# Optimization experiments

Hardware: AMD Instinct MI355X
Metric: run time of the kernel (lower is better)

The kernel has to match this reference:

```python
import jax, jax.numpy as jnp
import numpy as np

B, N, C, R = 16, 1024, 256, 8
E = 262144
NUM_SUPER = 32
EPS = 1e-5


def _ln(x, g, b):
    mu = jnp.mean(x, axis=-1, keepdims=True)
    var = jnp.var(x, axis=-1, keepdims=True)
    return (x - mu) / jnp.sqrt(var + EPS) * g + b


def setup_inputs() -> dict:
    key = jax.random.key(0)
    ks = jax.random.split(key, 20)

    def w(k, shape, fan_in):
        return (jax.random.normal(k, shape, jnp.float32) / np.sqrt(fan_in)).astype(jnp.float32)

    return dict(
        x=jax.random.normal(ks[0], (B, N, C), jnp.float32),
        batch_edge_index=jax.random.randint(ks[1], (2, E), 0, B * N),
        batch_edge_types=jax.random.randint(ks[2], (E,), 0, R),
        # cross-modal attention
        Wq=w(ks[3], (C, C), C), bq=jnp.zeros((C,), jnp.float32),
        Wk=w(ks[4], (C, C), C), bk=jnp.zeros((C,), jnp.float32),
        Wv=w(ks[5], (C, C), C), bv=jnp.zeros((C,), jnp.float32),
        Wg=w(ks[6], (2 * C, C), 2 * C), bg=jnp.zeros((C,), jnp.float32),
        ln_attn_g=jnp.ones((C,), jnp.float32), ln_attn_b=jnp.zeros((C,), jnp.float32),
        # confidence net
        Wc1=w(ks[7], (C, C // 2), C), bc1=jnp.zeros((C // 2,), jnp.float32),
        Wc2=w(ks[8], (C // 2, 1), C // 2), bc2=jnp.zeros((1,), jnp.float32),
        # feature mixer
        Wm=w(ks[9], (2 * C, C), 2 * C), bm=jnp.zeros((C,), jnp.float32),
        ln1_g=jnp.ones((C,), jnp.float32), ln1_b=jnp.zeros((C,), jnp.float32),
        # RGCN
        W_rel=w(ks[10], (R, C, C), C),
        W_root=w(ks[11], (C, C), C),
        b_rgcn=jnp.zeros((C,), jnp.float32),
        ln2_g=jnp.ones((C,), jnp.float32), ln2_b=jnp.zeros((C,), jnp.float32),
        # super class head
        Wh=w(ks[12], (C, NUM_SUPER), C), bh=jnp.zeros((NUM_SUPER,), jnp.float32),
    )


def reference(x, batch_edge_index, batch_edge_types,
              Wq, bq, Wk, bk, Wv, bv, Wg, bg, ln_attn_g, ln_attn_b,
              Wc1, bc1, Wc2, bc2, Wm, bm, ln1_g, ln1_b,
              W_rel, W_root, b_rgcn, ln2_g, ln2_b, Wh, bh):
    residual = x
    q = x @ Wq + bq
    k = x @ Wk + bk
    v = x @ Wv + bv
    attn = jax.nn.softmax(jnp.einsum('bnc,bmc->bnm', q, k) / jnp.sqrt(jnp.float32(C)), axis=-1)
    out = jnp.einsum('bnm,bmc->bnc', attn, v)
    gate = jax.nn.sigmoid(jnp.concatenate([out, residual], axis=-1) @ Wg + bg)
    validated = _ln(gate * out + (1.0 - gate) * residual, ln_attn_g, ln_attn_b)

    conf = jax.nn.sigmoid(jax.nn.relu(validated @ Wc1 + bc1) @ Wc2 + bc2)  # [B,N,1]
    weighted = validated * conf
    xm = jax.nn.relu(jnp.concatenate([x, weighted], axis=-1) @ Wm + bm)
    xn = _ln(xm, ln1_g, ln1_b).reshape(B * N, C)

    # RGCNConv (PyG defaults: mean aggregation per relation, root weight, bias)
    src, dst = batch_edge_index[0], batch_edge_index[1]
    h = jnp.einsum('nc,rcd->rnd', xn, W_rel)          # [R, B*N, C] relation-transformed nodes
    msg = h[batch_edge_types, src]                    # [E, C] per-edge gather
    seg = dst * R + batch_edge_types                  # (node, relation) segment id
    cnt = jax.ops.segment_sum(jnp.ones((E,), xn.dtype), seg, num_segments=B * N * R)
    msg = msg / jnp.maximum(cnt[seg], 1.0)[:, None]
    agg = jax.ops.segment_sum(msg, dst, num_segments=B * N)
    x_rgcn = agg + xn @ W_root + b_rgcn
    x_rgcn = jax.nn.relu(_ln(x_rgcn.reshape(B, N, C), ln2_g, ln2_b))

    denom = jnp.maximum(conf.sum(axis=1), 1e-8)       # [B,1]
    pooled = (x_rgcn * conf).sum(axis=1) / denom      # [B,C]
    return pooled @ Wh + bh                           # [B, NUM_SUPER]
```

## Files before the change

### kernel.cpp

```cpp
#include <hip/hip_runtime.h>
#include <hip/hip_bf16.h>

#define B_ 16
#define N_ 1024
#define C_ 256
#define R_ 8
#define E_ 262144
#define NS_ 32
#define BN_ (B_*N_)
#define BNC_ (BN_*C_)

typedef __hip_bfloat16 bf16;
typedef __attribute__((ext_vector_type(4))) float f32x4;
typedef __attribute__((ext_vector_type(8))) short bf16x8;

__device__ __forceinline__ float b2f(bf16 x) { return __bfloat162float(x); }
__device__ __forceinline__ bf16  f2b(float x) { return __float2bfloat16(x); }
__device__ __forceinline__ float us2f(unsigned short u) { return __uint_as_float((unsigned)u << 16); }

__device__ __forceinline__ void gload16(const void* g, void* l) {
    auto gp = (const __attribute__((address_space(1))) void*)(unsigned long long)g;
    auto lp = (__attribute__((address_space(3))) void*)(unsigned)(unsigned long long)l;
    __builtin_amdgcn_global_load_lds(gp, lp, 16, 0, 0);
}

template<int ACT>
__global__ __launch_bounds__(256) void gemm_bf16(
    const bf16* __restrict__ A, int lda, long long sA,
    const bf16* __restrict__ Bm, int ldb, long long sB,
    bf16* __restrict__ Cc, int ldc, long long sC,
    const float* __restrict__ bias, const float* __restrict__ bias2,
    const float* __restrict__ bias3, int K)
{
    __shared__ short sbuf[16384];
    const int tid = threadIdx.x;
    const int lane = tid & 63, w = tid >> 6;
    const int wr = w >> 1, wc = w & 1;

    const int gx = gridDim.x;
    const int nwg = gx * gridDim.y;
    int id = blockIdx.y * gx + blockIdx.x;
    if ((nwg & 7) == 0) { const int cpx = nwg >> 3; id = (id & 7) * cpx + (id >> 3); }
    const int bm = (id / gx) * 128, bn = (id % gx) * 128;

    const bf16* Ab = A + (size_t)blockIdx.z * sA;
    const bf16* Bb = Bm + (size_t)blockIdx.z * sB;
    bf16* Cb = Cc + (size_t)blockIdx.z * sC;

    const int rg = lane >> 2;
    const int kswz = ((lane & 3) ^ ((rg >> 1) & 3)) * 8;

    f32x4 acc[4][4];
    const f32x4 zz = {0.f, 0.f, 0.f, 0.f};
    #pragma unroll
    for (int i = 0; i < 4; ++i)
        #pragma unroll
        for (int j = 0; j < 4; ++j) acc[i][j] = zz;

    const int fr = lane & 15;
    const int fm = lane >> 4;
    const int fslot = (fm ^ ((fr >> 1) & 3)) * 8;

    const int NI = K >> 5;

#define STAGE_AB(bi, kk) do {                                                          \
    _Pragma("unroll")                                                                  \
    for (int t_ = 0; t_ < 2; ++t_) {                                                   \
        gload16(Ab + (size_t)(bm + t_*64 + w*16 + rg) * lda + (kk) + kswz,             \
                sbuf + (bi)*4096 + t_*2048 + w*512);                                   \
        gload16(Bb + (size_t)(bn + t_*64 + w*16 + rg) * ldb + (kk) + kswz,             \
                sbuf + 8192 + (bi)*4096 + t_*2048 + w*512);                            \
    } } while (0)

    STAGE_AB(0, 0);
    if (NI > 1) STAGE_AB(1, 32);

    for (int i = 0; i < NI; ++i) {
        const int cur = i & 1;
        if (i + 1 < NI) asm volatile("s_waitcnt vmcnt(4)" ::: "memory");
        else            asm volatile("s_waitcnt vmcnt(0)" ::: "memory");
        __builtin_amdgcn_s_barrier();
        __builtin_amdgcn_sched_barrier(0);

        bf16x8 af[4], bfr[4];
        const short* Ac = sbuf + cur * 4096;
        const short* Bc = sbuf + 8192 + cur * 4096;
        #pragma unroll
        for (int ii = 0; ii < 4; ++ii)
            af[ii] = *(const bf16x8*)&Ac[(wr*64 + ii*16 + fr)*32 + fslot];
        #pragma unroll
        for (int jj = 0; jj < 4; ++jj)
            bfr[jj] = *(const bf16x8*)&Bc[(wc*64 + jj*16 + fr)*32 + fslot];

        asm volatile("s_waitcnt lgkmcnt(0)" ::: "memory");
        __builtin_amdgcn_s_barrier();
        __builtin_amdgcn_sched_barrier(0);
        if (i + 2 < NI) STAGE_AB(cur, (i + 2) * 32);

        #pragma unroll
        for (int ii = 0; ii < 4; ++ii)
            #pragma unroll
            for (int jj = 0; jj < 4; ++jj)
                acc[ii][jj] = __builtin_amdgcn_mfma_f32_16x16x32_bf16(af[ii], bfr[jj], acc[ii][jj], 0, 0, 0);
    }
#undef STAGE_AB

    __syncthreads();
    const int er = (lane >> 4) * 4, ec = lane & 15;
    #pragma unroll
    for (int half = 0; half < 2; ++half) {
        if (wr == half) {
            #pragma unroll
            for (int j = 0; j < 4; ++j) {
                const int col = bn + wc*64 + j*16 + ec;
                float bvv = 0.0f;
                if (bias) {
                    const int seg = col >> 8;
                    const float* bp = (seg == 0) ? bias : (seg == 1 ? bias2 : bias3);
                    bvv = bp[col & 255];
                }
                #pragma unroll
                for (int i = 0; i < 4; ++i) {
                    #pragma unroll
                    for (int p = 0; p < 4; ++p) {
                        float val = acc[i][j][p] + bvv;
                        if (ACT == 1) val = fmaxf(val, 0.0f);
                        if (ACT == 2) val = 1.0f / (1.0f + __expf(-val));
                        *(bf16*)&sbuf[(i*16 + er + p)*136 + wc*64 + j*16 + ec] = f2b(val);
                    }
                }
            }
        }
        __syncthreads();
        #pragma unroll
        for (int it = 0; it < 4; ++it) {
            const int ch = tid + it*256;
            const int row = ch >> 4, cp = (ch & 15) * 8;
            *(bf16x8*)&Cb[(size_t)(bm + half*64 + row) * ldc + bn + cp] =
                *(const bf16x8*)&sbuf[row*136 + cp];
        }
        __syncthreads();
    }
}

template<int ACT>
__global__ __launch_bounds__(256) void gemm64_bf16(
    const bf16* __restrict__ A, int lda, long long sA,
    const bf16* __restrict__ Bm, int ldb, long long sB,
    bf16* __restrict__ Cc, int ldc, long long sC,
    const float* __restrict__ bias, int K)
{
    __shared__ short sbuf[16384];
    const int tid = threadIdx.x;
    const int lane = tid & 63, w = tid >> 6;
    const int wr = w >> 1, wc = w & 1;

    const int gx = gridDim.x;
    const int nwg = gx * gridDim.y;
    int id = blockIdx.y * gx + blockIdx.x;
    if ((nwg & 7) == 0) { const int cpx = nwg >> 3; id = (id & 7) * cpx + (id >> 3); }
    const int bm = (id / gx) * 64, bn = (id % gx) * 64;

    const bf16* Ab = A + (size_t)blockIdx.z * sA;
    const bf16* Bb = Bm + (size_t)blockIdx.z * sB;
    bf16* Cb = Cc + (size_t)blockIdx.z * sC;

    const int rg = lane >> 2;
    const int kswz = ((lane & 3) ^ ((rg >> 1) & 3)) * 8;

    f32x4 acc[2][2];
    const f32x4 zz = {0.f, 0.f, 0.f, 0.f};
    #pragma unroll
    for (int i = 0; i < 2; ++i)
        #pragma unroll
        for (int j = 0; j < 2; ++j) acc[i][j] = zz;

    const int fr = lane & 15;
    const int fm = lane >> 4;
    const int fslot = (fm ^ ((fr >> 1) & 3)) * 8;

    const int NI = K >> 5;

#define STAGE64(bi, kk) do {                                                           \
    gload16(Ab + (size_t)(bm + w*16 + rg) * lda + (kk) + kswz,                         \
            sbuf + (bi)*2048 + w*512);                                                 \
    gload16(Bb + (size_t)(bn + w*16 + rg) * ldb + (kk) + kswz,                         \
            sbuf + 8192 + (bi)*2048 + w*512);                                          \
    } while (0)

    STAGE64(0, 0);
    if (NI > 1) STAGE64(1, 32);
    if (NI > 2) STAGE64(2, 64);
    if (NI > 3) STAGE64(3, 96);

    for (int i = 0; i < NI; ++i) {
        const int cur = i & 3;
        if (i + 3 < NI)      asm volatile("s_waitcnt vmcnt(6)" ::: "memory");
        else if (i + 2 < NI) asm volatile("s_waitcnt vmcnt(4)" ::: "memory");
        else if (i + 1 < NI) asm volatile("s_waitcnt vmcnt(2)" ::: "memory");
        else                 asm volatile("s_waitcnt vmcnt(0)" ::: "memory");
        __builtin_amdgcn_s_barrier();
        __builtin_amdgcn_sched_barrier(0);

        bf16x8 af[2], bfr[2];
        const short* Ac = sbuf + cur * 2048;
        const short* Bc = sbuf + 8192 + cur * 2048;
        #pragma unroll
        for (int ii = 0; ii < 2; ++ii)
            af[ii] = *(const bf16x8*)&Ac[(wr*32 + ii*16 + fr)*32 + fslot];
        #pragma unroll
        for (int jj = 0; jj < 2; ++jj)
            bfr[jj] = *(const bf16x8*)&Bc[(wc*32 + jj*16 + fr)*32 + fslot];

        asm volatile("s_waitcnt lgkmcnt(0)" ::: "memory");
        __builtin_amdgcn_s_barrier();
        __builtin_amdgcn_sched_barrier(0);
        if (i + 4 < NI) STAGE64(cur, (i + 4) * 32);

        #pragma unroll
        for (int ii = 0; ii < 2; ++ii)
            #pragma unroll
            for (int jj = 0; jj < 2; ++jj)
                acc[ii][jj] = __builtin_amdgcn_mfma_f32_16x16x32_bf16(af[ii], bfr[jj], acc[ii][jj], 0, 0, 0);
    }
#undef STAGE64

    __syncthreads();
    const int er = (lane >> 4) * 4, ec = lane & 15;
    #pragma unroll
    for (int j = 0; j < 2; ++j) {
        const int col = bn + wc*32 + j*16 + ec;
        const float bvv = bias ? bias[col & 255] : 0.0f;
        #pragma unroll
        for (int i = 0; i < 2; ++i) {
            #pragma unroll
            for (int p = 0; p < 4; ++p) {
                float val = acc[i][j][p] + bvv;
                if (ACT == 1) val = fmaxf(val, 0.0f);
                if (ACT == 2) val = 1.0f / (1.0f + __expf(-val));
                *(bf16*)&sbuf[(wr*32 + i*16 + er + p)*72 + wc*32 + j*16 + ec] = f2b(val);
            }
        }
    }
    __syncthreads();
    #pragma unroll
    for (int it = 0; it < 2; ++it) {
        const int ch = tid + it*256;
        const int row = ch >> 3, cp = (ch & 7) * 8;
        *(bf16x8*)&Cb[(size_t)(bm + row) * ldc + bn + cp] =
            *(const bf16x8*)&sbuf[row*72 + cp];
    }
}

__global__ __launch_bounds__(256) void prep_w_k(
    const float* __restrict__ Wq, const float* __restrict__ Wk, const float* __restrict__ Wv,
    const float* __restrict__ Wg, const float* __restrict__ Wm, const float* __restrict__ Wc1,
    const float* __restrict__ Wrel, const float* __restrict__ Wroot, bf16* __restrict__ WT)
{
    int t = blockIdx.x;
    const float* in; bf16* out; int K, Nn;
    if (t < 192)      { int wsel = t >> 6; t &= 63;
                        in = wsel == 0 ? Wq : (wsel == 1 ? Wk : Wv);
                        out = WT + wsel*65536; K = 256; Nn = 256; }
    else if (t < 320) { t -= 192; in = Wg;  out = WT + 196608; K = 512; Nn = 256; }
    else if (t < 448) { t -= 320; in = Wm;  out = WT + 327680; K = 512; Nn = 256; }
    else if (t < 480) { t -= 448; in = Wc1; out = WT + 458752; K = 256; Nn = 128; }
    else if (t < 992) { t -= 480; int r = t >> 6; t &= 63;
                        in = Wrel + (size_t)r*65536; out = WT + 491520 + r*65536; K = 256; Nn = 256; }
    else              { t -= 992; in = Wroot; out = WT + 491520 + 524288; K = 256; Nn = 256; }
    const int tpr = Nn >> 5;
    const int n0 = (t % tpr) * 32, k0 = (t / tpr) * 32;
    __shared__ float tile[32][33];
    const int tx = threadIdx.x & 31, ty = threadIdx.x >> 5;
    #pragma unroll
    for (int i = 0; i < 4; ++i) {
        int r = ty + i*8;
        tile[r][tx] = in[(size_t)(k0 + r) * Nn + n0 + tx];
    }
    __syncthreads();
    #pragma unroll
    for (int i = 0; i < 4; ++i) {
        int r = ty + i*8;
        out[(size_t)(n0 + r) * K + k0 + tx] = f2b(tile[tx][r]);
    }
}

__global__ __launch_bounds__(256) void vtrans_k(
    const bf16* __restrict__ in, bf16* __restrict__ out)
{
    __shared__ float tile[32][33];
    in  += (size_t)blockIdx.z * 786432 + 512;
    out += (size_t)blockIdx.z * 262144;
    const int n0 = blockIdx.x * 32, k0 = blockIdx.y * 32;
    const int tx = threadIdx.x & 31, ty = threadIdx.x >> 5;
    #pragma unroll
    for (int i = 0; i < 4; ++i) {
        int r = ty + i*8;
        tile[r][tx] = b2f(in[(size_t)(k0 + r) * 768 + n0 + tx]);
    }
    __syncthreads();
    #pragma unroll
    for (int i = 0; i < 4; ++i) {
        int r = ty + i*8;
        out[(size_t)(n0 + r) * 1024 + k0 + tx] = f2b(tile[tx][r]);
    }
}

__global__ __launch_bounds__(256) void cvt_x_k(const float* __restrict__ x,
    bf16* __restrict__ xb, bf16* __restrict__ cat1, bf16* __restrict__ cat2)
{
    const int i4 = (blockIdx.x * 256 + threadIdx.x) * 4;
    const float4 xv = *(const float4*)(x + i4);
    bf16 bv[4] = { f2b(xv.x), f2b(xv.y), f2b(xv.z), f2b(xv.w) };
    const ushort4 pack = *(const ushort4*)bv;
    const int row = i4 >> 8, col = i4 & 255;
    *(ushort4*)(xb + i4) = pack;
    *(ushort4*)(cat1 + (size_t)row * 512 + 256 + col) = pack;
    *(ushort4*)(cat2 + (size_t)row * 512 + col) = pack;
}

__global__ __launch_bounds__(256) void softmax_k(bf16* __restrict__ s)
{
    const int row = blockIdx.x, tid = threadIdx.x;
    const int lane = tid & 63, wid = tid >> 6;
    bf16* rp = s + (size_t)row * 1024 + tid * 4;
    __shared__ float red[8];
    const ushort4 sv = *(const ushort4*)rp;
    float v0 = us2f(sv.x) * 0.0625f, v1 = us2f(sv.y) * 0.0625f;
    float v2 = us2f(sv.z) * 0.0625f, v3 = us2f(sv.w) * 0.0625f;
    float m = fmaxf(fmaxf(v0, v1), fmaxf(v2, v3));
    #pragma unroll
    for (int o = 32; o >= 1; o >>= 1) m = fmaxf(m, __shfl_xor(m, o));
    if (lane == 0) red[wid] = m;
    __syncthreads();
    const float mx = fmaxf(fmaxf(red[0], red[1]), fmaxf(red[2], red[3]));
    float e0 = __expf(v0 - mx), e1 = __expf(v1 - mx), e2 = __expf(v2 - mx), e3 = __expf(v3 - mx);
    float sm = e0 + e1 + e2 + e3;
    #pragma unroll
    for (int o = 32; o >= 1; o >>= 1) sm += __shfl_xor(sm, o);
    if (lane == 0) red[4 + wid] = sm;
    __syncthreads();
    const float inv = 1.0f / (red[4] + red[5] + red[6] + red[7]);
    bf16 ov[4] = { f2b(e0 * inv), f2b(e1 * inv), f2b(e2 * inv), f2b(e3 * inv) };
    *(ushort4*)rp = *(const ushort4*)ov;
}

template<int RELU>
__global__ __launch_bounds__(256) void ln_k(
    const bf16* __restrict__ in, bf16* __restrict__ out,
    const float* __restrict__ g, const float* __restrict__ bta)
{
    const int node = blockIdx.x * 4 + (threadIdx.x >> 6);
    const int lane = threadIdx.x & 63;
    const ushort4 iv = *(const ushort4*)(in + (size_t)node * 256 + lane * 4);
    float v0 = us2f(iv.x), v1 = us2f(iv.y), v2 = us2f(iv.z), v3 = us2f(iv.w);
    float s  = v0 + v1 + v2 + v3;
    float sq = v0*v0 + v1*v1 + v2*v2 + v3*v3;
    #pragma unroll
    for (int o = 32; o >= 1; o >>= 1) { s += __shfl_xor(s, o); sq += __shfl_xor(sq, o); }
    const float mean = s * (1.0f / 256.0f);
    const float var  = sq * (1.0f / 256.0f) - mean * mean;
    const float rs = rsqrtf(var + 1e-5f);
    const float4 gv = *(const float4*)(g + lane * 4);
    const float4 bv = *(const float4*)(bta + lane * 4);
    float y0 = (v0 - mean) * rs * gv.x + bv.x;
    float y1 = (v1 - mean) * rs * gv.y + bv.y;
    float y2 = (v2 - mean) * rs * gv.z + bv.z;
    float y3 = (v3 - mean) * rs * gv.w + bv.w;
    if (RELU) { y0 = fmaxf(y0, 0.f); y1 = fmaxf(y1, 0.f); y2 = fmaxf(y2, 0.f); y3 = fmaxf(y3, 0.f); }
    bf16 ov[4] = { f2b(y0), f2b(y1), f2b(y2), f2b(y3) };
    *(ushort4*)(out + (size_t)node * 256 + lane * 4) = *(const ushort4*)ov;
}

__global__ __launch_bounds__(256) void blend_ln_k(
    const bf16* __restrict__ gate, const bf16* __restrict__ cat1,
    const float* __restrict__ x, bf16* __restrict__ valid,
    const float* __restrict__ g, const float* __restrict__ bta)
{
    const int node = blockIdx.x * 4 + (threadIdx.x >> 6);
    const int lane = threadIdx.x & 63;
    const ushort4 gt4 = *(const ushort4*)(gate + (size_t)node * 256 + lane * 4);
    const ushort4 ao4 = *(const ushort4*)(cat1 + (size_t)node * 512 + lane * 4);
    const float4  xv4 = *(const float4*)(x + (size_t)node * 256 + lane * 4);
    float g0 = us2f(gt4.x), g1 = us2f(gt4.y), g2 = us2f(gt4.z), g3 = us2f(gt4.w);
    float v0 = g0 * us2f(ao4.x) + (1.f - g0) * xv4.x;
    float v1 = g1 * us2f(ao4.y) + (1.f - g1) * xv4.y;
    float v2 = g2 * us2f(ao4.z) + (1.f - g2) * xv4.z;
    float v3 = g3 * us2f(ao4.w) + (1.f - g3) * xv4.w;
    float s  = v0 + v1 + v2 + v3;
    float sq = v0*v0 + v1*v1 + v2*v2 + v3*v3;
    #pragma unroll
    for (int o = 32; o >= 1; o >>= 1) { s += __shfl_xor(s, o); sq += __shfl_xor(sq, o); }
    const float mean = s * (1.0f / 256.0f);
    const float var  = sq * (1.0f / 256.0f) - mean * mean;
    const float rs = rsqrtf(var + 1e-5f);
    const float4 gv = *(const float4*)(g + lane * 4);
    const float4 bv = *(const float4*)(bta + lane * 4);
    bf16 ov[4] = { f2b((v0 - mean) * rs * gv.x + bv.x), f2b((v1 - mean) * rs * gv.y + bv.y),
                   f2b((v2 - mean) * rs * gv.z + bv.z), f2b((v3 - mean) * rs * gv.w + bv.w) };
    *(ushort4*)(valid + (size_t)node * 256 + lane * 4) = *(const ushort4*)ov;
}

__global__ __launch_bounds__(256) void conf_w_k(
    const bf16* __restrict__ t1, const float* __restrict__ Wc2, const float* __restrict__ bc2,
    const bf16* __restrict__ valid, float* __restrict__ conf, bf16* __restrict__ cat2)
{
    const int node = blockIdx.x * 4 + (threadIdx.x >> 6);
    const int lane = threadIdx.x & 63;
    float a = b2f(t1[(size_t)node * 128 + lane]) * Wc2[lane]
            + b2f(t1[(size_t)node * 128 + 64 + lane]) * Wc2[64 + lane];
    #pragma unroll
    for (int o = 32; o >= 1; o >>= 1) a += __shfl_xor(a, o);
    const float c = 1.0f / (1.0f + __expf(-(a + bc2[0])));
    if (lane == 0) conf[node] = c;
    const ushort4 vv = *(const ushort4*)(valid + (size_t)node * 256 + lane * 4);
    bf16 ov[4] = { f2b(us2f(vv.x) * c), f2b(us2f(vv.y) * c), f2b(us2f(vv.z) * c), f2b(us2f(vv.w) * c) };
    *(ushort4*)(cat2 + (size_t)node * 512 + 256 + lane * 4) = *(const ushort4*)ov;
}

__global__ __launch_bounds__(256) void count2_k(
    const int* __restrict__ dst, const int* __restrict__ et,
    int* __restrict__ deg, int* __restrict__ cnt8)
{
    const int e = blockIdx.x * 256 + threadIdx.x;
    if (e < E_) {
        const int d = dst[e];
        atomicAdd(&deg[d], 1);
        atomicAdd(&cnt8[d * 8 + et[e]], 1);
    }
}

__global__ __launch_bounds__(256) void scan_k(
    const int* __restrict__ deg, int* __restrict__ rowptr, int* __restrict__ cursor)
{
    __shared__ int part[256];
    const int tid = threadIdx.x;
    const int base = tid * 64;
    int s = 0;
    for (int i = 0; i < 64; ++i) s += deg[base + i];
    part[tid] = s; __syncthreads();
    for (int off = 1; off < 256; off <<= 1) {
        int t = (tid >= off) ? part[tid - off] : 0;
        __syncthreads();
        part[tid] += t;
        __syncthreads();
    }
    int run = (tid == 0) ? 0 : part[tid - 1];
    for (int i = 0; i < 64; ++i) {
        rowptr[base + i] = run;
        cursor[base + i] = run;
        run += deg[base + i];
    }
    if (tid == 255) rowptr[BN_] = run;
}

__global__ __launch_bounds__(256) void fill_k(
    const int* __restrict__ src, const int* __restrict__ dst, const int* __restrict__ et,
    int* __restrict__ cursor, int* __restrict__ elist)
{
    const int e = blockIdx.x * 256 + threadIdx.x;
    if (e < E_) {
        const int pos = atomicAdd(&cursor[dst[e]], 1);
        elist[pos] = src[e] | (et[e] << 16);
    }
}

__global__ __launch_bounds__(256) void gather_ln_k(
    const int* __restrict__ rowptr, const int* __restrict__ elist,
    const bf16* __restrict__ h, const int* __restrict__ cnt8,
    const float* __restrict__ brg,
    const float* __restrict__ g, const float* __restrict__ bta,
    bf16* __restrict__ xr)
{
    const int node = blockIdx.x * 4 + (threadIdx.x >> 6);
    const int lane = threadIdx.x & 63;
    const int e0 = rowptr[node], e1 = rowptr[node + 1];
    float invc[8];
    #pragma unroll
    for (int r = 0; r < 8; ++r)
        invc[r] = 1.0f / fmaxf((float)cnt8[node * 8 + r], 1.0f);
    float a0 = 0.f, a1 = 0.f, a2 = 0.f, a3 = 0.f;
    int e = e0;
    for (; e + 1 < e1; e += 2) {
        const int pe0 = elist[e], pe1 = elist[e + 1];
        const float w0 = invc[pe0 >> 16], w1 = invc[pe1 >> 16];
        const ushort4 hv0 = *(const ushort4*)(h + (size_t)(pe0 & 0xffff) * 2304 + (pe0 >> 16) * 256 + lane * 4);
        const ushort4 hv1 = *(const ushort4*)(h + (size_t)(pe1 & 0xffff) * 2304 + (pe1 >> 16) * 256 + lane * 4);
        a0 += w0 * us2f(hv0.x) + w1 * us2f(hv1.x);
        a1 += w0 * us2f(hv0.y) + w1 * us2f(hv1.y);
        a2 += w0 * us2f(hv0.z) + w1 * us2f(hv1.z);
        a3 += w0 * us2f(hv0.w) + w1 * us2f(hv1.w);
    }
    if (e < e1) {
        const int pe = elist[e];
        const float wgt = invc[pe >> 16];
        const ushort4 hv = *(const ushort4*)(h + (size_t)(pe & 0xffff) * 2304 + (pe >> 16) * 256 + lane * 4);
        a0 += wgt * us2f(hv.x); a1 += wgt * us2f(hv.y);
        a2 += wgt * us2f(hv.z); a3 += wgt * us2f(hv.w);
    }
    const ushort4 rv = *(const ushort4*)(h + (size_t)node * 2304 + 2048 + lane * 4);
    const float4 bg4 = *(const float4*)(brg + lane * 4);
    const float v0 = a0 + us2f(rv.x) + bg4.x, v1 = a1 + us2f(rv.y) + bg4.y;
    const float v2 = a2 + us2f(rv.z) + bg4.z, v3 = a3 + us2f(rv.w) + bg4.w;
    float s  = v0 + v1 + v2 + v3;
    float sq = v0*v0 + v1*v1 + v2*v2 + v3*v3;
    #pragma unroll
    for (int m = 32; m >= 1; m >>= 1) { s += __shfl_xor(s, m); sq += __shfl_xor(sq, m); }
    const float mean = s * (1.0f / 256.0f);
    const float var  = sq * (1.0f / 256.0f) - mean * mean;
    const float rs = rsqrtf(var + 1e-5f);
    const float4 gv = *(const float4*)(g + lane * 4);
    const float4 bv = *(const float4*)(bta + lane * 4);
    bf16 tb[4] = { f2b(fmaxf((v0 - mean) * rs * gv.x + bv.x, 0.f)),
                   f2b(fmaxf((v1 - mean) * rs * gv.y + bv.y, 0.f)),
                   f2b(fmaxf((v2 - mean) * rs * gv.z + bv.z, 0.f)),
                   f2b(fmaxf((v3 - mean) * rs * gv.w + bv.w, 0.f)) };
    *(ushort4*)(xr + (size_t)node * 256 + lane * 4) = *(const ushort4*)tb;
}

__global__ __launch_bounds__(256) void pool1_k(
    const bf16* __restrict__ xr, const float* __restrict__ conf, float* __restrict__ partial)
{
    const int b = blockIdx.x, chunk = blockIdx.y, c = threadIdx.x;
    float acc = 0.0f;
    for (int n = 0; n < 64; ++n) {
        const int node = b * 1024 + chunk * 64 + n;
        acc += conf[node] * b2f(xr[(size_t)node * 256 + c]);
    }
    partial[(size_t)(b * 16 + chunk) * 256 + c] = acc;
}

__global__ __launch_bounds__(256) void pool2_k(
    const float* __restrict__ partial, const float* __restrict__ conf,
    const float* __restrict__ Wh, const float* __restrict__ bh, float* __restrict__ out)
{
    const int b = blockIdx.x, tid = threadIdx.x;
    __shared__ float red[256];
    __shared__ float pooled[256];
    float pc = 0.0f;
    for (int ch = 0; ch < 16; ++ch) pc += partial[(size_t)(b * 16 + ch) * 256 + tid];
    float s = conf[b * 1024 + tid] + conf[b * 1024 + 256 + tid]
            + conf[b * 1024 + 512 + tid] + conf[b * 1024 + 768 + tid];
    red[tid] = s; __syncthreads();
    for (int st = 128; st > 0; st >>= 1) { if (tid < st) red[tid] += red[tid + st]; __syncthreads(); }
    const float denom = fmaxf(red[0], 1e-8f);
    pooled[tid] = pc / denom;
    __syncthreads();
    if (tid < NS_) {
        float o = bh[tid];
        for (int c = 0; c < 256; ++c) o += pooled[c] * Wh[c * NS_ + tid];
        out[b * NS_ + tid] = o;
    }
}

extern "C" void kernel_launch(void* const* d_in, const int* in_sizes, int n_in,
                              void* d_out, int out_size, void* d_ws, size_t ws_size,
                              hipStream_t stream) {
    const float* x    = (const float*)d_in[0];
    const int*   ei   = (const int*)d_in[1];
    const int*   et   = (const int*)d_in[2];
    const float* Wq   = (const float*)d_in[3];  const float* bq  = (const float*)d_in[4];
    const float* Wk   = (const float*)d_in[5];  const float* bk  = (const float*)d_in[6];
    const float* Wv   = (const float*)d_in[7];  const float* bv  = (const float*)d_in[8];
    const float* Wg   = (const float*)d_in[9];  const float* bg  = (const float*)d_in[10];
    const float* lag  = (const float*)d_in[11]; const float* lab = (const float*)d_in[12];
    const float* Wc1  = (const float*)d_in[13]; const float* bc1 = (const float*)d_in[14];
    const float* Wc2  = (const float*)d_in[15]; const float* bc2 = (const float*)d_in[16];
    const float* Wm   = (const float*)d_in[17]; const float* bm  = (const float*)d_in[18];
    const float* l1g  = (const float*)d_in[19]; const float* l1b = (const float*)d_in[20];
    const float* Wrel = (const float*)d_in[21]; const float* Wroot = (const float*)d_in[22];
    const float* brg  = (const float*)d_in[23];
    const float* l2g  = (const float*)d_in[24]; const float* l2b = (const float*)d_in[25];
    const float* Wh   = (const float*)d_in[26]; const float* bh  = (const float*)d_in[27];
    const int* esrc = ei;
    const int* edst = ei + E_;

    char* w8 = (char*)d_ws;
    bf16*  qkv   = (bf16*)(w8 + 0);
    bf16*  hbuf  = (bf16*)(w8 + 0);
    bf16*  sP    = (bf16*)(w8 + 25165824);
    bf16*  cat1  = (bf16*)(w8 + 58720256);
    bf16*  cat2  = (bf16*)(w8 + 75497472);
    bf16*  gate  = (bf16*)(w8 + 92274688);
    bf16*  valid = (bf16*)(w8 + 100663296);
    bf16*  t1    = (bf16*)(w8 + 109051904);
    bf16*  xm    = (bf16*)(w8 + 113246208);
    bf16*  xb    = (bf16*)(w8 + 121634816);
    bf16*  xn    = (bf16*)(w8 + 130023424);
    bf16*  vtb   = (bf16*)(w8 + 138412032);
    bf16*  xr    = (bf16*)(w8 + 146800640);
    float* conf  = (float*)(w8 + 155189248);
    float* part  = (float*)(w8 + 155254784);
    bf16*  WT    = (bf16*)(w8 + 155516928);
    int*  deg    = (int*)(w8 + 157679616);
    int*  cnt8i  = (int*)(w8 + 157745152);
    int*  rowptr = (int*)(w8 + 158269440);
    int*  cursor = (int*)(w8 + 158335232);
    int*  elist  = (int*)(w8 + 158400768);
    bf16* WqkvT = WT;
    bf16* WgT   = WT + 196608;
    bf16* WmT   = WT + 327680;
    bf16* Wc1T  = WT + 458752;
    bf16* WBIG  = WT + 491520;
    float* outp = (float*)d_out;

    dim3 blk(256);

    prep_w_k<<<1056, blk, 0, stream>>>(Wq, Wk, Wv, Wg, Wm, Wc1, Wrel, Wroot, WT);
    cvt_x_k<<<BNC_ / 1024, blk, 0, stream>>>(x, xb, cat1, cat2);
    hipMemsetAsync(deg, 0, 589824, stream);
    count2_k<<<E_ / 256, blk, 0, stream>>>(edst, et, deg, cnt8i);
    scan_k<<<1, blk, 0, stream>>>(deg, rowptr, cursor);
    fill_k<<<E_ / 256, blk, 0, stream>>>(esrc, edst, et, cursor, elist);

    gemm_bf16<0><<<dim3(6, 128, 1), blk, 0, stream>>>(
        xb, 256, 0, WqkvT, 256, 0, qkv, 768, 0, bq, bk, bv, 256);
    vtrans_k<<<dim3(8, 32, 16), blk, 0, stream>>>(qkv, vtb);

    gemm_bf16<0><<<dim3(8, 8, 16), blk, 0, stream>>>(
        qkv, 768, 786432, qkv + 256, 768, 786432, sP, 1024, 1048576, nullptr, nullptr, nullptr, 256);
    softmax_k<<<BN_, blk, 0, stream>>>(sP);
    gemm_bf16<0><<<dim3(2, 8, 16), blk, 0, stream>>>(
        sP, 1024, 1048576, vtb, 1024, 262144, cat1, 512, 524288, nullptr, nullptr, nullptr, 1024);

    gemm64_bf16<2><<<dim3(4, 256, 1), blk, 0, stream>>>(
        cat1, 512, 0, WgT, 512, 0, gate, 256, 0, bg, 512);
    blend_ln_k<<<BN_ / 4, blk, 0, stream>>>(gate, cat1, x, valid, lag, lab);

    gemm64_bf16<1><<<dim3(2, 256, 1), blk, 0, stream>>>(
        valid, 256, 0, Wc1T, 256, 0, t1, 128, 0, bc1, 256);
    conf_w_k<<<BN_ / 4, blk, 0, stream>>>(t1, Wc2, bc2, valid, conf, cat2);

    gemm64_bf16<1><<<dim3(4, 256, 1), blk, 0, stream>>>(
        cat2, 512, 0, WmT, 512, 0, xm, 256, 0, bm, 512);
    ln_k<0><<<BN_ / 4, blk, 0, stream>>>(xm, xn, l1g, l1b);

    gemm_bf16<0><<<dim3(18, 128, 1), blk, 0, stream>>>(
        xn, 256, 0, WBIG, 256, 0, hbuf, 2304, 0, nullptr, nullptr, nullptr, 256);
    gather_ln_k<<<BN_ / 4, blk, 0, stream>>>(rowptr, elist, hbuf, cnt8i, brg, l2g, l2b, xr);

    pool1_k<<<dim3(B_, 16), blk, 0, stream>>>(xr, conf, part);
    pool2_k<<<B_, blk, 0, stream>>>(part, conf, Wh, bh, outp);
}
```

Measured before the change: 263.8 us.

## Triple-buffer 128x128 GEMM, unroll gather by four, read bf16 residual

The 128-tile GEMM moves from double to triple buffering in LDS. Three k-tiles are now in flight, with matching vmcnt waits and a rotating buffer index, to hide more global load latency. The edge gather loop is unrolled from two to four edges so more independent loads are outstanding per iteration. blend_ln_k now reads the bf16 copy of x instead of the fp32 input, which halves those bytes but uses a lower-precision residual. The larger LDS footprint (48KB) may reduce occupancy of the GEMM.

```diff
diff --git a/kernel.cpp b/kernel.cpp
--- a/kernel.cpp
+++ b/kernel.cpp
@@ -32,7 +32,7 @@
     const float* __restrict__ bias, const float* __restrict__ bias2,
     const float* __restrict__ bias3, int K)
 {
-    __shared__ short sbuf[16384];
+    __shared__ short sbuf[24576];
     const int tid = threadIdx.x;
     const int lane = tid & 63, w = tid >> 6;
     const int wr = w >> 1, wc = w & 1;
@@ -69,22 +69,24 @@
         gload16(Ab + (size_t)(bm + t_*64 + w*16 + rg) * lda + (kk) + kswz,             \
                 sbuf + (bi)*4096 + t_*2048 + w*512);                                   \
         gload16(Bb + (size_t)(bn + t_*64 + w*16 + rg) * ldb + (kk) + kswz,             \
-                sbuf + 8192 + (bi)*4096 + t_*2048 + w*512);                            \
+                sbuf + 12288 + (bi)*4096 + t_*2048 + w*512);                           \
     } } while (0)
 
     STAGE_AB(0, 0);
     if (NI > 1) STAGE_AB(1, 32);
-
+    if (NI > 2) STAGE_AB(2, 64);
+
+    int cur = 0;
     for (int i = 0; i < NI; ++i) {
-        const int cur = i & 1;
-        if (i + 1 < NI) asm volatile("s_waitcnt vmcnt(4)" ::: "memory");
-        else            asm volatile("s_waitcnt vmcnt(0)" ::: "memory");
+        if (i + 2 < NI)      asm volatile("s_waitcnt vmcnt(8)" ::: "memory");
+        else if (i + 1 < NI) asm volatile("s_waitcnt vmcnt(4)" ::: "memory");
+        else                 asm volatile("s_waitcnt vmcnt(0)" ::: "memory");
         __builtin_amdgcn_s_barrier();
         __builtin_amdgcn_sched_barrier(0);
 
         bf16x8 af[4], bfr[4];
         const short* Ac = sbuf + cur * 4096;
-        const short* Bc = sbuf + 8192 + cur * 4096;
+        const short* Bc = sbuf + 12288 + cur * 4096;
         #pragma unroll
         for (int ii = 0; ii < 4; ++ii)
             af[ii] = *(const bf16x8*)&Ac[(wr*64 + ii*16 + fr)*32 + fslot];
@@ -95,13 +97,14 @@
         asm volatile("s_waitcnt lgkmcnt(0)" ::: "memory");
         __builtin_amdgcn_s_barrier();
         __builtin_amdgcn_sched_barrier(0);
-        if (i + 2 < NI) STAGE_AB(cur, (i + 2) * 32);
+        if (i + 3 < NI) STAGE_AB(cur, (i + 3) * 32);
 
         #pragma unroll
         for (int ii = 0; ii < 4; ++ii)
             #pragma unroll
             for (int jj = 0; jj < 4; ++jj)
                 acc[ii][jj] = __builtin_amdgcn_mfma_f32_16x16x32_bf16(af[ii], bfr[jj], acc[ii][jj], 0, 0, 0);
+        cur = (cur == 2) ? 0 : cur + 1;
     }
 #undef STAGE_AB
 
@@ -204,7 +207,7 @@
 
         bf16x8 af[2], bfr[2];
         const short* Ac = sbuf + cur * 2048;
-        const short* Bc = sbuf + 8192 + cur * 2048;
+        const short* Bc = sbuf + 4096*2 + cur * 2048;
         #pragma unroll
         for (int ii = 0; ii < 2; ++ii)
             af[ii] = *(const bf16x8*)&Ac[(wr*32 + ii*16 + fr)*32 + fslot];
@@ -374,19 +377,19 @@
 
 __global__ __launch_bounds__(256) void blend_ln_k(
     const bf16* __restrict__ gate, const bf16* __restrict__ cat1,
-    const float* __restrict__ x, bf16* __restrict__ valid,
+    const bf16* __restrict__ xb, bf16* __restrict__ valid,
     const float* __restrict__ g, const float* __restrict__ bta)
 {
     const int node = blockIdx.x * 4 + (threadIdx.x >> 6);
     const int lane = threadIdx.x & 63;
     const ushort4 gt4 = *(const ushort4*)(gate + (size_t)node * 256 + lane * 4);
     const ushort4 ao4 = *(const ushort4*)(cat1 + (size_t)node * 512 + lane * 4);
-    const float4  xv4 = *(const float4*)(x + (size_t)node * 256 + lane * 4);
+    const ushort4 xv4 = *(const ushort4*)(xb + (size_t)node * 256 + lane * 4);
     float g0 = us2f(gt4.x), g1 = us2f(gt4.y), g2 = us2f(gt4.z), g3 = us2f(gt4.w);
-    float v0 = g0 * us2f(ao4.x) + (1.f - g0) * xv4.x;
-    float v1 = g1 * us2f(ao4.y) + (1.f - g1) * xv4.y;
-    float v2 = g2 * us2f(ao4.z) + (1.f - g2) * xv4.z;
-    float v3 = g3 * us2f(ao4.w) + (1.f - g3) * xv4.w;
+    float v0 = g0 * us2f(ao4.x) + (1.f - g0) * us2f(xv4.x);
+    float v1 = g1 * us2f(ao4.y) + (1.f - g1) * us2f(xv4.y);
+    float v2 = g2 * us2f(ao4.z) + (1.f - g2) * us2f(xv4.z);
+    float v3 = g3 * us2f(ao4.w) + (1.f - g3) * us2f(xv4.w);
     float s  = v0 + v1 + v2 + v3;
     float sq = v0*v0 + v1*v1 + v2*v2 + v3*v3;
     #pragma unroll
@@ -481,17 +484,20 @@
         invc[r] = 1.0f / fmaxf((float)cnt8[node * 8 + r], 1.0f);
     float a0 = 0.f, a1 = 0.f, a2 = 0.f, a3 = 0.f;
     int e = e0;
-    for (; e + 1 < e1; e += 2) {
-        const int pe0 = elist[e], pe1 = elist[e + 1];
-        const float w0 = invc[pe0 >> 16], w1 = invc[pe1 >> 16];
-        const ushort4 hv0 = *(const ushort4*)(h + (size_t)(pe0 & 0xffff) * 2304 + (pe0 >> 16) * 256 + lane * 4);
-        const ushort4 hv1 = *(const ushort4*)(h + (size_t)(pe1 & 0xffff) * 2304 + (pe1 >> 16) * 256 + lane * 4);
-        a0 += w0 * us2f(hv0.x) + w1 * us2f(hv1.x);
-        a1 += w0 * us2f(hv0.y) + w1 * us2f(hv1.y);
-        a2 += w0 * us2f(hv0.z) + w1 * us2f(hv1.z);
-        a3 += w0 * us2f(hv0.w) + w1 * us2f(hv1.w);
-    }
-    if (e < e1) {
+    for (; e + 3 < e1; e += 4) {
+        const int p0 = elist[e], p1 = elist[e+1], p2 = elist[e+2], p3 = elist[e+3];
+        const float w0 = invc[p0 >> 16], w1 = invc[p1 >> 16];
+        const float w2 = invc[p2 >> 16], w3 = invc[p3 >> 16];
+        const ushort4 h0 = *(const ushort4*)(h + (size_t)(p0 & 0xffff) * 2304 + (p0 >> 16) * 256 + lane * 4);
+        const ushort4 h1 = *(const ushort4*)(h + (size_t)(p1 & 0xffff) * 2304 + (p1 >> 16) * 256 + lane * 4);
+        const ushort4 h2 = *(const ushort4*)(h + (size_t)(p2 & 0xffff) * 2304 + (p2 >> 16) * 256 + lane * 4);
+        const ushort4 h3 = *(const ushort4*)(h + (size_t)(p3 & 0xffff) * 2304 + (p3 >> 16) * 256 + lane * 4);
+        a0 += w0 * us2f(h0.x) + w1 * us2f(h1.x) + w2 * us2f(h2.x) + w3 * us2f(h3.x);
+        a1 += w0 * us2f(h0.y) + w1 * us2f(h1.y) + w2 * us2f(h2.y) + w3 * us2f(h3.y);
+        a2 += w0 * us2f(h0.z) + w1 * us2f(h1.z) + w2 * us2f(h2.z) + w3 * us2f(h3.z);
+        a3 += w0 * us2f(h0.w) + w1 * us2f(h1.w) + w2 * us2f(h2.w) + w3 * us2f(h3.w);
+    }
+    for (; e < e1; ++e) {
         const int pe = elist[e];
         const float wgt = invc[pe >> 16];
         const ushort4 hv = *(const ushort4*)(h + (size_t)(pe & 0xffff) * 2304 + (pe >> 16) * 256 + lane * 4);
@@ -625,7 +631,7 @@
 
     gemm64_bf16<2><<<dim3(4, 256, 1), blk, 0, stream>>>(
         cat1, 512, 0, WgT, 512, 0, gate, 256, 0, bg, 512);
-    blend_ln_k<<<BN_ / 4, blk, 0, stream>>>(gate, cat1, x, valid, lag, lab);
+    blend_ln_k<<<BN_ / 4, blk, 0, stream>>>(gate, cat1, xb, valid, lag, lab);
 
     gemm64_bf16<1><<<dim3(2, 256, 1), blk, 0, stream>>>(
         valid, 256, 0, Wc1T, 256, 0, t1, 128, 0, bc1, 256);
```

Result: no change. 261.2 us (-1.0%).
